# Performance work log

Hardware: AMD Instinct MI355X
Metric: run time of the kernel (lower is better)

## Reference

```python
import jax, jax.numpy as jnp
import numpy as np

WH, WW = 7, 7           # window height/width
N = WH * WW             # tokens per window = 49
C = 768                 # num_channels
H = 24                  # num_heads
D = C // H              # head_dim = 32
B = 1024                # total windows (batch * windows-per-image)
NW = 64                 # windows per image (shift_mask leading dim)
EPS = 1e-5


def _relative_position_index():
    # Mirrors the torch buffer construction in __init__.
    coords = np.stack(np.meshgrid(np.arange(WH), np.arange(WW), indexing='ij'))  # [2,WH,WW]
    cf = coords.reshape(2, -1)                          # [2,N]
    rel = cf[:, :, None] - cf[:, None, :]               # [2,N,N]
    rel = rel.transpose(1, 2, 0).copy()                 # [N,N,2]
    rel[:, :, 0] += WH - 1
    rel[:, :, 1] += WW - 1
    rel[:, :, 0] *= 2 * WW - 1
    return jnp.asarray(rel.sum(-1), dtype=jnp.int32)    # [N,N]


def setup_inputs() -> dict:
    key = jax.random.key(0)
    ks = jax.random.split(key, 6)
    x = jax.random.normal(ks[0], (B, N, C), dtype=jnp.float32)
    shift_mask = jax.random.normal(ks[1], (NW, N, N), dtype=jnp.float32)
    w_qkv = jax.random.normal(ks[2], (3 * C, C), dtype=jnp.float32) * 0.02
    b_qkv = jnp.zeros((3 * C,), dtype=jnp.float32)
    w_proj = jax.random.normal(ks[3], (C, C), dtype=jnp.float32) * 0.02
    b_proj = jnp.zeros((C,), dtype=jnp.float32)
    rel_bias_table = jax.random.normal(ks[4], ((2 * WH - 1) * (2 * WW - 1), H), dtype=jnp.float32) * 0.02
    ln_g = jnp.ones((C,), dtype=jnp.float32)
    ln_b = jnp.zeros((C,), dtype=jnp.float32)
    rel_pos_index = _relative_position_index()
    return {
        'x': x, 'shift_mask': shift_mask,
        'w_qkv': w_qkv, 'b_qkv': b_qkv,
        'w_proj': w_proj, 'b_proj': b_proj,
        'rel_bias_table': rel_bias_table,
        'ln_g': ln_g, 'ln_b': ln_b,
        'rel_pos_index': rel_pos_index,
    }


def reference(x, shift_mask, w_qkv, b_qkv, w_proj, b_proj, rel_bias_table, ln_g, ln_b, rel_pos_index):
    B_, N_, C_ = x.shape
    # QKV projection: [B,N,3C] -> [3,B,H,N,D]
    qkv = (x @ w_qkv.T + b_qkv).reshape(B_, N_, 3, H, D).transpose(2, 0, 3, 1, 4)
    q, k, v = qkv[0], qkv[1], qkv[2]
    # Relative position bias gather: [N,N,H] -> [1,H,N,N]
    bias = rel_bias_table[rel_pos_index.reshape(-1)].reshape(N_, N_, H).transpose(2, 0, 1)[None]
    # Shift mask broadcast over batch repeats and heads: [B,1,N,N]
    mask = jnp.tile(shift_mask, (B_ // shift_mask.shape[0], 1, 1))[:, None]
    attn_bias = bias + mask  # [B,H,N,N]
    scale = 1.0 / np.sqrt(D).astype(np.float32)
    scores = jnp.einsum('bhnd,bhmd->bhnm', q, k) * scale + attn_bias
    attn = jax.nn.softmax(scores, axis=-1)
    out = jnp.einsum('bhnm,bhmd->bhnd', attn, v)       # [B,H,N,D]
    out = out.transpose(0, 2, 1, 3).reshape(B_, N_, C_)
    out = out @ w_proj.T + b_proj                      # dropout p=0 -> identity
    y = out + x
    mu = jnp.mean(y, axis=-1, keepdims=True)
    var = jnp.mean(jnp.square(y - mu), axis=-1, keepdims=True)
    return (y - mu) * jax.lax.rsqrt(var + EPS) * ln_g + ln_b
```

## Files before the change

### kernel.cpp

```cpp
#include <hip/hip_runtime.h>
#include <hip/hip_bf16.h>

#define SEQ 49
#define CH 768
#define NH 24
#define HD 32
#define NB 1024
#define NWIN 64
#define MTOT (NB*SEQ)
#define K3 (3*CH)

typedef __hip_bfloat16 bf16;
typedef __attribute__((ext_vector_type(8))) short short8;
typedef __attribute__((ext_vector_type(4))) short short4v;
typedef __attribute__((ext_vector_type(4))) float f32x4;

#define MD  ((size_t)MTOT * HD)
#define NHMD ((size_t)NH * MD)

__device__ __forceinline__ void gload16(const void* g, void* l) {
  __builtin_amdgcn_global_load_lds((__attribute__((address_space(1))) void*)g,
                                   (__attribute__((address_space(3))) void*)l,
                                   16, 0, 0);
}

__device__ __forceinline__ float bf2f(short s) {
  return __uint_as_float(((unsigned int)(unsigned short)s) << 16);
}

__global__ void cvt_bf16(const float* __restrict__ in, bf16* __restrict__ o, int n4) {
  int i = blockIdx.x * blockDim.x + threadIdx.x;
  if (i >= n4) return;
  float4 v = ((const float4*)in)[i];
  union { bf16 b[4]; short4 s; } u;
  u.b[0] = __float2bfloat16(v.x);
  u.b[1] = __float2bfloat16(v.y);
  u.b[2] = __float2bfloat16(v.z);
  u.b[3] = __float2bfloat16(v.w);
  ((short4*)o)[i] = u.s;
}

__global__ void build_comb(const float* __restrict__ table, const int* __restrict__ rpi,
                           const float* __restrict__ smask, float* __restrict__ comb) {
  int i = blockIdx.x * blockDim.x + threadIdx.x;
  if (i >= NWIN * NH * SEQ * SEQ) return;
  int mn = i % (SEQ * SEQ);
  int sh = i / (SEQ * SEQ);
  int h = sh % NH;
  int s = sh / NH;
  comb[i] = table[rpi[mn] * NH + h] + smask[s * SEQ * SEQ + mn];
}


__global__ __launch_bounds__(256) void qkv_gemm(
    const bf16* __restrict__ A, const bf16* __restrict__ Bw,
    const float* __restrict__ bias, bf16* __restrict__ C)
{
  __shared__ __align__(16) bf16 As[2 * 128 * 64];
  __shared__ __align__(16) bf16 Bs[2 * 128 * 64];
  const int tid = threadIdx.x;
  const int w = tid >> 6, l = tid & 63;
  const int lr = l & 15, lg = l >> 4;
  const int wm = w >> 1, wn = w & 1;

  const int flat = blockIdx.x;
  const int wg = (flat & 7) * 882 + (flat >> 3);
  const int bm = wg / 18, bn = wg - 18 * (wg / 18);

  const int srow0 = tid >> 3;
  const int chk = tid & 7;
  const bf16* gA[4];
  const bf16* gB[4];
#pragma unroll
  for (int j = 0; j < 4; j++) {
    int row = j * 32 + srow0;
    int srcch = chk ^ (row & 7);
    gA[j] = A + ((size_t)(bm * 128 + row)) * CH + srcch * 8;
    gB[j] = Bw + ((size_t)(bn * 128 + row)) * CH + srcch * 8;
  }

  f32x4 acc[4][4];
  f32x4 zero4 = {0.f, 0.f, 0.f, 0.f};
#pragma unroll
  for (int i = 0; i < 4; i++)
#pragma unroll
    for (int j = 0; j < 4; j++) acc[i][j] = zero4;

  int offA[4][2], offB[4][2];
#pragma unroll
  for (int mi = 0; mi < 4; mi++) {
#pragma unroll
    for (int ks = 0; ks < 2; ks++) {
      int rowa = 64 * wm + 16 * mi + lr;
      offA[mi][ks] = rowa * 64 + ((lg + 4 * ks) ^ (rowa & 7)) * 8;
      int rowb = 64 * wn + 16 * mi + lr;
      offB[mi][ks] = rowb * 64 + ((lg + 4 * ks) ^ (rowb & 7)) * 8;
    }
  }

#pragma unroll
  for (int j = 0; j < 4; j++) gload16(gA[j], As + j * 2048 + tid * 8);
#pragma unroll
  for (int j = 0; j < 4; j++) gload16(gB[j], Bs + j * 2048 + tid * 8);
  __syncthreads();

  int cur = 0;
  for (int t = 0; t < 12; ++t) {
    const bf16* cA = As + cur * 8192;
    const bf16* cB = Bs + cur * 8192;
    if (t < 11) {
      const int kk = (t + 1) * 64;
      bf16* nA = As + (cur ^ 1) * 8192;
      bf16* nB = Bs + (cur ^ 1) * 8192;
#pragma unroll
      for (int j = 0; j < 4; j++) gload16(gA[j] + kk, nA + j * 2048 + tid * 8);
#pragma unroll
      for (int j = 0; j < 4; j++) gload16(gB[j] + kk, nB + j * 2048 + tid * 8);
    }
    short8 af[4][2], bfv[4][2];
#pragma unroll
    for (int mi = 0; mi < 4; mi++)
#pragma unroll
      for (int ks = 0; ks < 2; ks++) {
        af[mi][ks] = *(const short8*)(cA + offA[mi][ks]);
        bfv[mi][ks] = *(const short8*)(cB + offB[mi][ks]);
      }
    __builtin_amdgcn_s_setprio(1);
#pragma unroll
    for (int ks = 0; ks < 2; ks++)
#pragma unroll
      for (int mi = 0; mi < 4; mi++)
#pragma unroll
        for (int nj = 0; nj < 4; nj++)
          acc[mi][nj] = __builtin_amdgcn_mfma_f32_16x16x32_bf16(af[mi][ks], bfv[nj][ks], acc[mi][nj], 0, 0, 0);
    __builtin_amdgcn_s_setprio(0);
    __syncthreads();
    cur ^= 1;
  }

  const int colbase = bn * 128 + 64 * wn;
  const int rowbase = bm * 128 + 64 * wm;
#pragma unroll
  for (int nj = 0; nj < 4; nj++) {
    const int cb16 = colbase + 16 * nj;
    const int sec = cb16 / 768;
    const int rem = cb16 - sec * 768;
    const int h = rem >> 5;
    const int dbase = rem & 31;
    float bv = bias[cb16 + lr];
    const size_t base = (size_t)sec * NHMD + (size_t)h * MD + dbase + lr;
#pragma unroll
    for (int mi = 0; mi < 4; mi++) {
#pragma unroll
      for (int r = 0; r < 4; r++) {
        size_t row = rowbase + 16 * mi + 4 * lg + r;
        C[base + row * HD] = __float2bfloat16(acc[mi][nj][r] + bv);
      }
    }
  }
}

__global__ __launch_bounds__(256) void attn_kernel(
    const bf16* __restrict__ qkvT, const float* __restrict__ comb,
    bf16* __restrict__ aout)
{
  __shared__ __align__(16) bf16 P[4][64 * 72];
  const int tid = threadIdx.x;
  const int w = tid >> 6, l = tid & 63;
  const int lr = l & 15, lg = l >> 4;
  const int b = blockIdx.x;
  const int h = blockIdx.y * 4 + w;
  const size_t rowb = (size_t)b * SEQ;
  const float scale = 0.17677669529663687f;
  f32x4 zero4 = {0.f, 0.f, 0.f, 0.f};

  const bf16* qb = qkvT + (size_t)h * MD + rowb * HD;
  const bf16* kb = qkvT + NHMD + (size_t)h * MD + rowb * HD;
  const bf16* vb = qkvT + 2 * NHMD + (size_t)h * MD + rowb * HD;

  short8 qf[4], kf[4];
#pragma unroll
  for (int mt = 0; mt < 4; mt++)
    qf[mt] = *(const short8*)(qb + (16 * mt + lr) * HD + 8 * lg);
#pragma unroll
  for (int nt = 0; nt < 4; nt++)
    kf[nt] = *(const short8*)(kb + (16 * nt + lr) * HD + 8 * lg);

  f32x4 s[4][4];
#pragma unroll
  for (int mt = 0; mt < 4; mt++)
#pragma unroll
    for (int nt = 0; nt < 4; nt++)
      s[mt][nt] = __builtin_amdgcn_mfma_f32_16x16x32_bf16(qf[mt], kf[nt], zero4, 0, 0, 0);

  const short* vs = (const short*)vb;
  short8 pb[2][2];
#pragma unroll
  for (int kt = 0; kt < 2; kt++)
#pragma unroll
    for (int dt = 0; dt < 2; dt++) {
      short8 t;
#pragma unroll
      for (int j = 0; j < 8; j++) {
        int n = 32 * kt + 8 * lg + j;
        short val = 0;
        if (n < SEQ) val = vs[n * HD + 16 * dt + lr];
        t[j] = val;
      }
      pb[kt][dt] = t;
    }

  const float* cb = comb + ((size_t)((b & (NWIN - 1)) * NH + h)) * (SEQ * SEQ);
#pragma unroll
  for (int mt = 0; mt < 4; mt++)
#pragma unroll
    for (int nt = 0; nt < 4; nt++)
#pragma unroll
      for (int r = 0; r < 4; r++) {
        int m = 16 * mt + 4 * lg + r, n = 16 * nt + lr;
        float v;
        if (m < SEQ && n < SEQ) v = s[mt][nt][r] * scale + cb[m * SEQ + n];
        else v = -1e30f;
        s[mt][nt][r] = v;
      }

  float mx[4][4];
#pragma unroll
  for (int mt = 0; mt < 4; mt++)
#pragma unroll
    for (int r = 0; r < 4; r++) {
      float m0 = fmaxf(fmaxf(s[mt][0][r], s[mt][1][r]), fmaxf(s[mt][2][r], s[mt][3][r]));
      m0 = fmaxf(m0, __shfl_xor(m0, 1, 64));
      m0 = fmaxf(m0, __shfl_xor(m0, 2, 64));
      m0 = fmaxf(m0, __shfl_xor(m0, 4, 64));
      m0 = fmaxf(m0, __shfl_xor(m0, 8, 64));
      mx[mt][r] = m0;
    }
  float inv[4][4];
#pragma unroll
  for (int mt = 0; mt < 4; mt++)
#pragma unroll
    for (int r = 0; r < 4; r++) {
      float t = 0.f;
#pragma unroll
      for (int nt = 0; nt < 4; nt++) {
        float e = __expf(s[mt][nt][r] - mx[mt][r]);
        s[mt][nt][r] = e;
        t += e;
      }
      t += __shfl_xor(t, 1, 64);
      t += __shfl_xor(t, 2, 64);
      t += __shfl_xor(t, 4, 64);
      t += __shfl_xor(t, 8, 64);
      inv[mt][r] = 1.0f / t;
    }

#pragma unroll
  for (int mt = 0; mt < 4; mt++)
#pragma unroll
    for (int nt = 0; nt < 4; nt++)
#pragma unroll
      for (int r = 0; r < 4; r++)
        P[w][(16 * mt + 4 * lg + r) * 72 + 16 * nt + lr] =
            __float2bfloat16(s[mt][nt][r] * inv[mt][r]);

  f32x4 o[4][2];
#pragma unroll
  for (int mt = 0; mt < 4; mt++) { o[mt][0] = zero4; o[mt][1] = zero4; }
#pragma unroll
  for (int kt = 0; kt < 2; kt++) {
    short8 pa[4];
#pragma unroll
    for (int mt = 0; mt < 4; mt++)
      pa[mt] = *(const short8*)(&P[w][(16 * mt + lr) * 72 + 32 * kt + 8 * lg]);
#pragma unroll
    for (int mt = 0; mt < 4; mt++)
#pragma unroll
      for (int dt = 0; dt < 2; dt++)
        o[mt][dt] = __builtin_amdgcn_mfma_f32_16x16x32_bf16(pa[mt], pb[kt][dt], o[mt][dt], 0, 0, 0);
  }

#pragma unroll
  for (int mt = 0; mt < 4; mt++)
#pragma unroll
    for (int dt = 0; dt < 2; dt++)
#pragma unroll
      for (int r = 0; r < 4; r++) {
        int m = 16 * mt + 4 * lg + r;
        if (m < SEQ)
          aout[(rowb + m) * CH + h * HD + 16 * dt + lr] = __float2bfloat16(o[mt][dt][r]);
      }
}

__global__ __launch_bounds__(256) void proj_gemm(
    const bf16* __restrict__ A, const bf16* __restrict__ Bw,
    const float* __restrict__ bias, const float* __restrict__ x,
    bf16* __restrict__ Y)
{
  __shared__ __align__(16) bf16 As[2 * 128 * 64];
  __shared__ __align__(16) bf16 Bs[2 * 128 * 64];
  const int tid = threadIdx.x;
  const int w = tid >> 6, l = tid & 63;
  const int lr = l & 15, lg = l >> 4;
  const int wm = w >> 1, wn = w & 1;

  const int flat = blockIdx.x;
  const int wg = (flat & 7) * 294 + (flat >> 3);
  const int bm = wg / 6, bn = wg - 6 * (wg / 6);

  const int srow0 = tid >> 3;
  const int chk = tid & 7;
  const bf16* gA[4];
  const bf16* gB[4];
#pragma unroll
  for (int j = 0; j < 4; j++) {
    int row = j * 32 + srow0;
    int srcch = chk ^ (row & 7);
    gA[j] = A + ((size_t)(bm * 128 + row)) * CH + srcch * 8;
    gB[j] = Bw + ((size_t)(bn * 128 + row)) * CH + srcch * 8;
  }

  f32x4 acc[4][4];
  f32x4 zero4 = {0.f, 0.f, 0.f, 0.f};
#pragma unroll
  for (int i = 0; i < 4; i++)
#pragma unroll
    for (int j = 0; j < 4; j++) acc[i][j] = zero4;

  int offA[4][2], offB[4][2];
#pragma unroll
  for (int mi = 0; mi < 4; mi++) {
#pragma unroll
    for (int ks = 0; ks < 2; ks++) {
      int rowa = 64 * wm + 16 * mi + lr;
      offA[mi][ks] = rowa * 64 + ((lg + 4 * ks) ^ (rowa & 7)) * 8;
      int rowb = 64 * wn + 16 * mi + lr;
      offB[mi][ks] = rowb * 64 + ((lg + 4 * ks) ^ (rowb & 7)) * 8;
    }
  }

#pragma unroll
  for (int j = 0; j < 4; j++) gload16(gA[j], As + j * 2048 + tid * 8);
#pragma unroll
  for (int j = 0; j < 4; j++) gload16(gB[j], Bs + j * 2048 + tid * 8);
  __syncthreads();

  int cur = 0;
  for (int t = 0; t < 12; ++t) {
    const bf16* cA = As + cur * 8192;
    const bf16* cB = Bs + cur * 8192;
    if (t < 11) {
      const int kk = (t + 1) * 64;
      bf16* nA = As + (cur ^ 1) * 8192;
      bf16* nB = Bs + (cur ^ 1) * 8192;
#pragma unroll
      for (int j = 0; j < 4; j++) gload16(gA[j] + kk, nA + j * 2048 + tid * 8);
#pragma unroll
      for (int j = 0; j < 4; j++) gload16(gB[j] + kk, nB + j * 2048 + tid * 8);
    }
    short8 af[4][2], bfv[4][2];
#pragma unroll
    for (int mi = 0; mi < 4; mi++)
#pragma unroll
      for (int ks = 0; ks < 2; ks++) {
        af[mi][ks] = *(const short8*)(cA + offA[mi][ks]);
        bfv[mi][ks] = *(const short8*)(cB + offB[mi][ks]);
      }
    __builtin_amdgcn_s_setprio(1);
#pragma unroll
    for (int ks = 0; ks < 2; ks++)
#pragma unroll
      for (int mi = 0; mi < 4; mi++)
#pragma unroll
        for (int nj = 0; nj < 4; nj++)
          acc[mi][nj] = __builtin_amdgcn_mfma_f32_16x16x32_bf16(af[mi][ks], bfv[nj][ks], acc[mi][nj], 0, 0, 0);
    __builtin_amdgcn_s_setprio(0);
    __syncthreads();
    cur ^= 1;
  }

  const int colbase = bn * 128 + 64 * wn;
  const int rowbase = bm * 128 + 64 * wm;
#pragma unroll
  for (int nj = 0; nj < 4; nj++) {
    int col = colbase + 16 * nj + lr;
    float bv = bias[col];
#pragma unroll
    for (int mi = 0; mi < 4; mi++) {
#pragma unroll
      for (int r = 0; r < 4; r++) {
        size_t row = rowbase + 16 * mi + 4 * lg + r;
        float v = acc[mi][nj][r] + bv + x[row * CH + col];
        Y[row * CH + col] = __float2bfloat16(v);
      }
    }
  }
}

__global__ __launch_bounds__(256) void ln_kernel(
    const bf16* __restrict__ Y, const float* __restrict__ g,
    const float* __restrict__ be, float* __restrict__ out)
{
  const int w = threadIdx.x >> 6, l = threadIdx.x & 63;
  const size_t r = (size_t)blockIdx.x * 4 + w;
  const bf16* yr = Y + r * CH;

  short8 a = *(const short8*)(yr + 8 * l);
  short4v b4 = *(const short4v*)(yr + 512 + 4 * l);
  float v[12];
#pragma unroll
  for (int j = 0; j < 8; j++) v[j] = bf2f(a[j]);
#pragma unroll
  for (int j = 0; j < 4; j++) v[8 + j] = bf2f(b4[j]);

  float s1 = 0.f, s2 = 0.f;
#pragma unroll
  for (int j = 0; j < 12; j++) { s1 += v[j]; s2 += v[j] * v[j]; }
#pragma unroll
  for (int m = 1; m <= 32; m <<= 1) {
    s1 += __shfl_xor(s1, m, 64);
    s2 += __shfl_xor(s2, m, 64);
  }
  float mu = s1 * (1.0f / 768.0f);
  float var = s2 * (1.0f / 768.0f) - mu * mu;
  float rs = rsqrtf(var + 1e-5f);

  float4 g0 = *(const float4*)(g + 8 * l);
  float4 g1 = *(const float4*)(g + 8 * l + 4);
  float4 g2 = *(const float4*)(g + 512 + 4 * l);
  float4 b0 = *(const float4*)(be + 8 * l);
  float4 b1 = *(const float4*)(be + 8 * l + 4);
  float4 b2 = *(const float4*)(be + 512 + 4 * l);

  float4 o0, o1, o2;
  o0.x = (v[0] - mu) * rs * g0.x + b0.x;
  o0.y = (v[1] - mu) * rs * g0.y + b0.y;
  o0.z = (v[2] - mu) * rs * g0.z + b0.z;
  o0.w = (v[3] - mu) * rs * g0.w + b0.w;
  o1.x = (v[4] - mu) * rs * g1.x + b1.x;
  o1.y = (v[5] - mu) * rs * g1.y + b1.y;
  o1.z = (v[6] - mu) * rs * g1.z + b1.z;
  o1.w = (v[7] - mu) * rs * g1.w + b1.w;
  o2.x = (v[8] - mu) * rs * g2.x + b2.x;
  o2.y = (v[9] - mu) * rs * g2.y + b2.y;
  o2.z = (v[10] - mu) * rs * g2.z + b2.z;
  o2.w = (v[11] - mu) * rs * g2.w + b2.w;

  float* orow = out + r * CH;
  *(float4*)(orow + 8 * l) = o0;
  *(float4*)(orow + 8 * l + 4) = o1;
  *(float4*)(orow + 512 + 4 * l) = o2;
}

extern "C" void kernel_launch(void* const* d_in, const int* in_sizes, int n_in,
                              void* d_out, int out_size, void* d_ws, size_t ws_size,
                              hipStream_t stream) {
  (void)in_sizes; (void)n_in; (void)out_size; (void)ws_size;
  const float* x     = (const float*)d_in[0];
  const float* smask = (const float*)d_in[1];
  const float* wqkv  = (const float*)d_in[2];
  const float* bqkv  = (const float*)d_in[3];
  const float* wproj = (const float*)d_in[4];
  const float* bproj = (const float*)d_in[5];
  const float* table = (const float*)d_in[6];
  const float* lng   = (const float*)d_in[7];
  const float* lnb   = (const float*)d_in[8];
  const int*   rpi   = (const int*)d_in[9];
  float* out = (float*)d_out;

  char* ws = (char*)d_ws;
  bf16*  xb   = (bf16*)(ws);
  bf16*  wqb  = (bf16*)(ws + 77070336);
  bf16*  wpb  = (bf16*)(ws + 80609280);
  float* comb = (float*)(ws + 81788928);
  bf16*  qkvT = (bf16*)(ws + 96534528);
  bf16*  aout = (bf16*)(ws + 327745536);
  bf16*  yb   = (bf16*)(ws + 96534528);

  cvt_bf16<<<37632, 256, 0, stream>>>(x, xb, 9633792);
  cvt_bf16<<<1728, 256, 0, stream>>>(wqkv, wqb, 442368);
  cvt_bf16<<<576, 256, 0, stream>>>(wproj, wpb, 147456);
  build_comb<<<14400, 256, 0, stream>>>(table, rpi, smask, comb);
  qkv_gemm<<<7056, 256, 0, stream>>>(xb, wqb, bqkv, qkvT);
  attn_kernel<<<dim3(1024, 6), 256, 0, stream>>>(qkvT, comb, aout);
  proj_gemm<<<2352, 256, 0, stream>>>(aout, wpb, bproj, x, yb);
  ln_kernel<<<12544, 256, 0, stream>>>(yb, lng, lnb, out);
}
```

Baseline: 593.5 us.

## Deepen GEMM prefetch, store V transposed, pad bias table, defer softmax normalization

Both GEMMs now issue loads two k-steps ahead, with explicit vmcnt waits and a barrier after the LDS reads, in place of a single prefetch followed by __syncthreads. The QKV epilogue folds the softmax scale into Q and writes V transposed so the attention kernel can load V fragments with vector loads instead of scalar gathers. The combined bias is padded to 64x64 with -1e30 baked into the padding, which removes the bounds checks and scale multiply from the attention kernel. Softmax normalization moves to after the PV product. The workspace layout is reshuffled and the padded table uses more memory.

Measured after the change: 603.8 us. About the same (+1.7%).

```diff
diff --git a/kernel.cpp b/kernel.cpp
--- a/kernel.cpp
+++ b/kernel.cpp
@@ -8,7 +8,6 @@
 #define NB 1024
 #define NWIN 64
 #define MTOT (NB*SEQ)
-#define K3 (3*CH)
 
 typedef __hip_bfloat16 bf16;
 typedef __attribute__((ext_vector_type(8))) short short8;
@@ -43,12 +42,15 @@
 __global__ void build_comb(const float* __restrict__ table, const int* __restrict__ rpi,
                            const float* __restrict__ smask, float* __restrict__ comb) {
   int i = blockIdx.x * blockDim.x + threadIdx.x;
-  if (i >= NWIN * NH * SEQ * SEQ) return;
-  int mn = i % (SEQ * SEQ);
-  int sh = i / (SEQ * SEQ);
+  int mn = i & 4095;
+  int m = mn >> 6, n = mn & 63;
+  int sh = i >> 12;
   int h = sh % NH;
   int s = sh / NH;
-  comb[i] = table[rpi[mn] * NH + h] + smask[s * SEQ * SEQ + mn];
+  float v = -1e30f;
+  if (m < SEQ && n < SEQ)
+    v = table[rpi[m * SEQ + n] * NH + h] + smask[s * SEQ * SEQ + m * SEQ + n];
+  comb[i] = v;
 }
 
 
@@ -67,16 +69,17 @@
   const int wg = (flat & 7) * 882 + (flat >> 3);
   const int bm = wg / 18, bn = wg - 18 * (wg / 18);
 
-  const int srow0 = tid >> 3;
-  const int chk = tid & 7;
   const bf16* gA[4];
   const bf16* gB[4];
+  int ldst[4];
 #pragma unroll
   for (int j = 0; j < 4; j++) {
-    int row = j * 32 + srow0;
-    int srcch = chk ^ (row & 7);
+    int c = j * 256 + tid;
+    int row = c >> 3, cpos = c & 7;
+    int srcch = cpos ^ (row & 7);
     gA[j] = A + ((size_t)(bm * 128 + row)) * CH + srcch * 8;
     gB[j] = Bw + ((size_t)(bn * 128 + row)) * CH + srcch * 8;
+    ldst[j] = c * 8;
   }
 
   f32x4 acc[4][4];
@@ -99,24 +102,22 @@
   }
 
 #pragma unroll
-  for (int j = 0; j < 4; j++) gload16(gA[j], As + j * 2048 + tid * 8);
-#pragma unroll
-  for (int j = 0; j < 4; j++) gload16(gB[j], Bs + j * 2048 + tid * 8);
-  __syncthreads();
-
-  int cur = 0;
+  for (int j = 0; j < 4; j++) gload16(gA[j], As + ldst[j]);
+#pragma unroll
+  for (int j = 0; j < 4; j++) gload16(gB[j], Bs + ldst[j]);
+#pragma unroll
+  for (int j = 0; j < 4; j++) gload16(gA[j] + 64, As + 8192 + ldst[j]);
+#pragma unroll
+  for (int j = 0; j < 4; j++) gload16(gB[j] + 64, Bs + 8192 + ldst[j]);
+
   for (int t = 0; t < 12; ++t) {
-    const bf16* cA = As + cur * 8192;
-    const bf16* cB = Bs + cur * 8192;
-    if (t < 11) {
-      const int kk = (t + 1) * 64;
-      bf16* nA = As + (cur ^ 1) * 8192;
-      bf16* nB = Bs + (cur ^ 1) * 8192;
-#pragma unroll
-      for (int j = 0; j < 4; j++) gload16(gA[j] + kk, nA + j * 2048 + tid * 8);
-#pragma unroll
-      for (int j = 0; j < 4; j++) gload16(gB[j] + kk, nB + j * 2048 + tid * 8);
-    }
+    if (t < 11) asm volatile("s_waitcnt vmcnt(8)" ::: "memory");
+    else        asm volatile("s_waitcnt vmcnt(0)" ::: "memory");
+    __builtin_amdgcn_sched_barrier(0);
+    __builtin_amdgcn_s_barrier();
+    const int base = (t & 1) * 8192;
+    const bf16* cA = As + base;
+    const bf16* cB = Bs + base;
     short8 af[4][2], bfv[4][2];
 #pragma unroll
     for (int mi = 0; mi < 4; mi++)
@@ -125,6 +126,16 @@
         af[mi][ks] = *(const short8*)(cA + offA[mi][ks]);
         bfv[mi][ks] = *(const short8*)(cB + offB[mi][ks]);
       }
+    asm volatile("s_waitcnt lgkmcnt(0)" ::: "memory");
+    __builtin_amdgcn_sched_barrier(0);
+    __builtin_amdgcn_s_barrier();
+    if (t < 10) {
+      const int kk = (t + 2) * 64;
+#pragma unroll
+      for (int j = 0; j < 4; j++) gload16(gA[j] + kk, As + base + ldst[j]);
+#pragma unroll
+      for (int j = 0; j < 4; j++) gload16(gB[j] + kk, Bs + base + ldst[j]);
+    }
     __builtin_amdgcn_s_setprio(1);
 #pragma unroll
     for (int ks = 0; ks < 2; ks++)
@@ -134,10 +145,9 @@
         for (int nj = 0; nj < 4; nj++)
           acc[mi][nj] = __builtin_amdgcn_mfma_f32_16x16x32_bf16(af[mi][ks], bfv[nj][ks], acc[mi][nj], 0, 0, 0);
     __builtin_amdgcn_s_setprio(0);
-    __syncthreads();
-    cur ^= 1;
-  }
-
+  }
+
+  const float scale = 0.17677669529663687f;
   const int colbase = bn * 128 + 64 * wn;
   const int rowbase = bm * 128 + 64 * wm;
 #pragma unroll
@@ -148,13 +158,26 @@
     const int h = rem >> 5;
     const int dbase = rem & 31;
     float bv = bias[cb16 + lr];
-    const size_t base = (size_t)sec * NHMD + (size_t)h * MD + dbase + lr;
-#pragma unroll
-    for (int mi = 0; mi < 4; mi++) {
-#pragma unroll
-      for (int r = 0; r < 4; r++) {
-        size_t row = rowbase + 16 * mi + 4 * lg + r;
-        C[base + row * HD] = __float2bfloat16(acc[mi][nj][r] + bv);
+    if (sec == 2) {
+      const size_t vbase = 2 * NHMD + ((size_t)h * HD + dbase + lr) * MTOT;
+#pragma unroll
+      for (int mi = 0; mi < 4; mi++) {
+        size_t row = rowbase + 16 * mi + 4 * lg;
+        union { bf16 b[4]; short4 s; } u;
+#pragma unroll
+        for (int r = 0; r < 4; r++) u.b[r] = __float2bfloat16(acc[mi][nj][r] + bv);
+        *(short4*)(C + vbase + row) = u.s;
+      }
+    } else {
+      const float mul = (sec == 0) ? scale : 1.0f;
+      const size_t base = (size_t)sec * NHMD + (size_t)h * MD + dbase + lr;
+#pragma unroll
+      for (int mi = 0; mi < 4; mi++) {
+#pragma unroll
+        for (int r = 0; r < 4; r++) {
+          size_t row = rowbase + 16 * mi + 4 * lg + r;
+          C[base + row * HD] = __float2bfloat16((acc[mi][nj][r] + bv) * mul);
+        }
       }
     }
   }
@@ -171,12 +194,11 @@
   const int b = blockIdx.x;
   const int h = blockIdx.y * 4 + w;
   const size_t rowb = (size_t)b * SEQ;
-  const float scale = 0.17677669529663687f;
   f32x4 zero4 = {0.f, 0.f, 0.f, 0.f};
 
   const bf16* qb = qkvT + (size_t)h * MD + rowb * HD;
   const bf16* kb = qkvT + NHMD + (size_t)h * MD + rowb * HD;
-  const bf16* vb = qkvT + 2 * NHMD + (size_t)h * MD + rowb * HD;
+  const bf16* vT = qkvT + 2 * NHMD + (size_t)h * HD * MTOT;
 
   short8 qf[4], kf[4];
 #pragma unroll
@@ -193,36 +215,21 @@
     for (int nt = 0; nt < 4; nt++)
       s[mt][nt] = __builtin_amdgcn_mfma_f32_16x16x32_bf16(qf[mt], kf[nt], zero4, 0, 0, 0);
 
-  const short* vs = (const short*)vb;
   short8 pb[2][2];
 #pragma unroll
   for (int kt = 0; kt < 2; kt++)
 #pragma unroll
-    for (int dt = 0; dt < 2; dt++) {
-      short8 t;
-#pragma unroll
-      for (int j = 0; j < 8; j++) {
-        int n = 32 * kt + 8 * lg + j;
-        short val = 0;
-        if (n < SEQ) val = vs[n * HD + 16 * dt + lr];
-        t[j] = val;
-      }
-      pb[kt][dt] = t;
-    }
-
-  const float* cb = comb + ((size_t)((b & (NWIN - 1)) * NH + h)) * (SEQ * SEQ);
+    for (int dt = 0; dt < 2; dt++)
+      pb[kt][dt] = *(const short8*)(vT + ((size_t)(16 * dt + lr)) * MTOT + rowb + 32 * kt + 8 * lg);
+
+  const float* cb = comb + (((size_t)(b & (NWIN - 1)) * NH + h) << 12);
 #pragma unroll
   for (int mt = 0; mt < 4; mt++)
 #pragma unroll
     for (int nt = 0; nt < 4; nt++)
 #pragma unroll
-      for (int r = 0; r < 4; r++) {
-        int m = 16 * mt + 4 * lg + r, n = 16 * nt + lr;
-        float v;
-        if (m < SEQ && n < SEQ) v = s[mt][nt][r] * scale + cb[m * SEQ + n];
-        else v = -1e30f;
-        s[mt][nt][r] = v;
-      }
+      for (int r = 0; r < 4; r++)
+        s[mt][nt][r] += cb[((16 * mt + 4 * lg + r) << 6) + 16 * nt + lr];
 
   float mx[4][4];
 #pragma unroll
@@ -262,7 +269,7 @@
 #pragma unroll
       for (int r = 0; r < 4; r++)
         P[w][(16 * mt + 4 * lg + r) * 72 + 16 * nt + lr] =
-            __float2bfloat16(s[mt][nt][r] * inv[mt][r]);
+            __float2bfloat16(s[mt][nt][r]);
 
   f32x4 o[4][2];
 #pragma unroll
@@ -288,7 +295,8 @@
       for (int r = 0; r < 4; r++) {
         int m = 16 * mt + 4 * lg + r;
         if (m < SEQ)
-          aout[(rowb + m) * CH + h * HD + 16 * dt + lr] = __float2bfloat16(o[mt][dt][r]);
+          aout[(rowb + m) * CH + h * HD + 16 * dt + lr] =
+              __float2bfloat16(o[mt][dt][r] * inv[mt][r]);
       }
 }
 
@@ -308,16 +316,17 @@
   const int wg = (flat & 7) * 294 + (flat >> 3);
   const int bm = wg / 6, bn = wg - 6 * (wg / 6);
 
-  const int srow0 = tid >> 3;
-  const int chk = tid & 7;
   const bf16* gA[4];
   const bf16* gB[4];
+  int ldst[4];
 #pragma unroll
   for (int j = 0; j < 4; j++) {
-    int row = j * 32 + srow0;
-    int srcch = chk ^ (row & 7);
+    int c = j * 256 + tid;
+    int row = c >> 3, cpos = c & 7;
+    int srcch = cpos ^ (row & 7);
     gA[j] = A + ((size_t)(bm * 128 + row)) * CH + srcch * 8;
     gB[j] = Bw + ((size_t)(bn * 128 + row)) * CH + srcch * 8;
+    ldst[j] = c * 8;
   }
 
   f32x4 acc[4][4];
@@ -340,24 +349,22 @@
   }
 
 #pragma unroll
-  for (int j = 0; j < 4; j++) gload16(gA[j], As + j * 2048 + tid * 8);
-#pragma unroll
-  for (int j = 0; j < 4; j++) gload16(gB[j], Bs + j * 2048 + tid * 8);
-  __syncthreads();
-
-  int cur = 0;
+  for (int j = 0; j < 4; j++) gload16(gA[j], As + ldst[j]);
+#pragma unroll
+  for (int j = 0; j < 4; j++) gload16(gB[j], Bs + ldst[j]);
+#pragma unroll
+  for (int j = 0; j < 4; j++) gload16(gA[j] + 64, As + 8192 + ldst[j]);
+#pragma unroll
+  for (int j = 0; j < 4; j++) gload16(gB[j] + 64, Bs + 8192 + ldst[j]);
+
   for (int t = 0; t < 12; ++t) {
-    const bf16* cA = As + cur * 8192;
-    const bf16* cB = Bs + cur * 8192;
-    if (t < 11) {
-      const int kk = (t + 1) * 64;
-      bf16* nA = As + (cur ^ 1) * 8192;
-      bf16* nB = Bs + (cur ^ 1) * 8192;
-#pragma unroll
-      for (int j = 0; j < 4; j++) gload16(gA[j] + kk, nA + j * 2048 + tid * 8);
-#pragma unroll
-      for (int j = 0; j < 4; j++) gload16(gB[j] + kk, nB + j * 2048 + tid * 8);
-    }
+    if (t < 11) asm volatile("s_waitcnt vmcnt(8)" ::: "memory");
+    else        asm volatile("s_waitcnt vmcnt(0)" ::: "memory");
+    __builtin_amdgcn_sched_barrier(0);
+    __builtin_amdgcn_s_barrier();
+    const int base = (t & 1) * 8192;
+    const bf16* cA = As + base;
+    const bf16* cB = Bs + base;
     short8 af[4][2], bfv[4][2];
 #pragma unroll
     for (int mi = 0; mi < 4; mi++)
@@ -366,6 +373,16 @@
         af[mi][ks] = *(const short8*)(cA + offA[mi][ks]);
         bfv[mi][ks] = *(const short8*)(cB + offB[mi][ks]);
       }
+    asm volatile("s_waitcnt lgkmcnt(0)" ::: "memory");
+    __builtin_amdgcn_sched_barrier(0);
+    __builtin_amdgcn_s_barrier();
+    if (t < 10) {
+      const int kk = (t + 2) * 64;
+#pragma unroll
+      for (int j = 0; j < 4; j++) gload16(gA[j] + kk, As + base + ldst[j]);
+#pragma unroll
+      for (int j = 0; j < 4; j++) gload16(gB[j] + kk, Bs + base + ldst[j]);
+    }
     __builtin_amdgcn_s_setprio(1);
 #pragma unroll
     for (int ks = 0; ks < 2; ks++)
@@ -375,8 +392,6 @@
         for (int nj = 0; nj < 4; nj++)
           acc[mi][nj] = __builtin_amdgcn_mfma_f32_16x16x32_bf16(af[mi][ks], bfv[nj][ks], acc[mi][nj], 0, 0, 0);
     __builtin_amdgcn_s_setprio(0);
-    __syncthreads();
-    cur ^= 1;
   }
 
   const int colbase = bn * 128 + 64 * wn;
@@ -473,14 +488,14 @@
   bf16*  wqb  = (bf16*)(ws + 77070336);
   bf16*  wpb  = (bf16*)(ws + 80609280);
   float* comb = (float*)(ws + 81788928);
-  bf16*  qkvT = (bf16*)(ws + 96534528);
-  bf16*  aout = (bf16*)(ws + 327745536);
-  bf16*  yb   = (bf16*)(ws + 96534528);
+  bf16*  qkvT = (bf16*)(ws + 106954752);
+  bf16*  aout = (bf16*)(ws);
+  bf16*  yb   = (bf16*)(ws + 106954752);
 
   cvt_bf16<<<37632, 256, 0, stream>>>(x, xb, 9633792);
   cvt_bf16<<<1728, 256, 0, stream>>>(wqkv, wqb, 442368);
   cvt_bf16<<<576, 256, 0, stream>>>(wproj, wpb, 147456);
-  build_comb<<<14400, 256, 0, stream>>>(table, rpi, smask, comb);
+  build_comb<<<24576, 256, 0, stream>>>(table, rpi, smask, comb);
   qkv_gemm<<<7056, 256, 0, stream>>>(xb, wqb, bqkv, qkvT);
   attn_kernel<<<dim3(1024, 6), 256, 0, stream>>>(qkvT, comb, aout);
   proj_gemm<<<2352, 256, 0, stream>>>(aout, wpb, bproj, x, yb);
```
